# Optimization experiments

Hardware: AMD Instinct MI355X
Metric: run time of the kernel (lower is better)

The kernel has to match this reference:

```python
import jax, jax.numpy as jnp
import numpy as np

NUM_HEADS = 8
NUM_POINTS = 4


def _grid_sample_bilinear(img, grid, H, W):
    """torch F.grid_sample(mode='bilinear', padding='zeros', align_corners=False).
    img:  [B, H, W, D]   grid: [B, S, 2] with (x, y) in [-1, 1].
    Returns [B, S, D].
    """
    gx, gy = grid[..., 0], grid[..., 1]
    # align_corners=False pixel mapping
    x = ((gx + 1.0) * W - 1.0) * 0.5
    y = ((gy + 1.0) * H - 1.0) * 0.5
    x0 = jnp.floor(x)
    y0 = jnp.floor(y)
    wx1 = x - x0
    wy1 = y - y0
    x0i = x0.astype(jnp.int32)
    y0i = y0.astype(jnp.int32)
    img_flat = img.reshape(img.shape[0], H * W, img.shape[-1])  # [B, N, D]

    def corner(xi, yi, w):
        valid = (xi >= 0) & (xi < W) & (yi >= 0) & (yi < H)  # zeros padding
        idx = jnp.clip(yi, 0, H - 1) * W + jnp.clip(xi, 0, W - 1)  # [B, S]
        v = jnp.take_along_axis(img_flat, idx[..., None], axis=1)  # [B, S, D]
        return v * (w * valid.astype(img.dtype))[..., None]

    out = corner(x0i, y0i, (1.0 - wx1) * (1.0 - wy1))
    out += corner(x0i + 1, y0i, wx1 * (1.0 - wy1))
    out += corner(x0i, y0i + 1, (1.0 - wx1) * wy1)
    out += corner(x0i + 1, y0i + 1, wx1 * wy1)
    return out


def setup_inputs() -> dict:
    key = jax.random.key(0)
    ks = jax.random.split(key, 12)
    B, Q, D = 4, 1024, 256
    H, W = 128, 128
    nh, npts = NUM_HEADS, NUM_POINTS
    f32 = jnp.float32
    return {
        "query": jax.random.normal(ks[0], (B, Q, D), f32),
        "reference_points": jax.random.uniform(ks[1], (B, Q, 2), f32),
        "value": jax.random.normal(ks[2], (B, H * W, D), f32),
        "W_off": jax.random.normal(ks[3], (D, nh * npts * 2), f32) * 0.02,
        "b_off": jax.random.normal(ks[4], (nh * npts * 2,), f32) * 0.02,
        "W_attn": jax.random.normal(ks[5], (D, nh * npts), f32) * 0.02,
        "b_attn": jax.random.normal(ks[6], (nh * npts,), f32) * 0.02,
        "W_v": jax.random.normal(ks[7], (D, D), f32) * (D ** -0.5),
        "b_v": jnp.zeros((D,), f32),
        "W_out": jax.random.normal(ks[8], (nh * D, D), f32) * ((nh * D) ** -0.5),
        "b_out": jnp.zeros((D,), f32),
        "H": H,
        "W": W,
    }


def reference(query, reference_points, value, W_off, b_off, W_attn, b_attn,
              W_v, b_v, W_out, b_out, H, W):
    B, Q, D = query.shape
    nh, npts = NUM_HEADS, NUM_POINTS
    # learned offsets and per-point attention weights
    offsets = (query @ W_off + b_off).reshape(B, Q, nh, npts, 2)
    attn = jax.nn.softmax((query @ W_attn + b_attn).reshape(B, Q, nh, npts), axis=-1)
    # sampling locations in [-1, 1]
    locs = reference_points[:, :, None, None, :] + offsets * 0.1
    locs = jnp.clip(locs, 0.0, 1.0) * 2.0 - 1.0
    # value projection -> 2D feature map [B, H, W, D]
    img = (value @ W_v + b_v).reshape(B, H, W, D)
    # sample all heads/points at once
    grid = locs.reshape(B, Q * nh * npts, 2)
    sampled = _grid_sample_bilinear(img, grid, H, W).reshape(B, Q, nh, npts, D)
    # weighted reduce over points, concat heads
    weighted = jnp.einsum("bqhpd,bqhp->bqhd", sampled, attn)
    out = weighted.reshape(B, Q, nh * D) @ W_out + b_out
    return out
```

## Files before the change

### kernel.cpp

```cpp
#include <hip/hip_runtime.h>
#include <hip/hip_bf16.h>
#include <math.h>

constexpr int B  = 4;
constexpr int Q  = 1024;
constexpr int D  = 256;
constexpr int NH = 8;
constexpr int NP = 4;
constexpr int H  = 128;
constexpr int W  = 128;
constexpr int HW = H * W;
constexpr int KAUG = 2112;

typedef short   bf16x8  __attribute__((ext_vector_type(8)));
typedef float   f32x4   __attribute__((ext_vector_type(4)));
typedef short   short4v __attribute__((ext_vector_type(4)));
typedef unsigned short ushort8v __attribute__((ext_vector_type(8)));

__device__ inline unsigned short f2bf(float f) {
    union { float f; unsigned u; } v; v.f = f;
    unsigned r = v.u + 0x7fff + ((v.u >> 16) & 1);
    return (unsigned short)(r >> 16);
}
__device__ inline float bf2f(unsigned short s) {
    union { unsigned u; float f; } v; v.u = ((unsigned)s) << 16;
    return v.f;
}

__device__ inline void async16(const void* g, void* l) {
    __builtin_amdgcn_global_load_lds(
        (const __attribute__((address_space(1))) unsigned*)g,
        (__attribute__((address_space(3))) unsigned*)l, 16, 0, 0);
}

constexpr int RB_CONV  = 0;
constexpr int RB_OFF   = RB_CONV  + (B * HW * D) / 1024;
constexpr int RB_CONVT = RB_OFF   + B * Q;
constexpr int RB_WV    = RB_CONVT + (NH * D * D) / 256;
constexpr int RB_BV    = RB_WV    + (D * D) / 1024;
constexpr int RB_END   = RB_BV    + (D * 64) / 256;

__global__ __launch_bounds__(256)
void k_prep(const float* __restrict__ value,
            const float* __restrict__ query,
            const float* __restrict__ refpts,
            const float* __restrict__ W_off,  const float* __restrict__ b_off,
            const float* __restrict__ W_attn, const float* __restrict__ b_attn,
            const float* __restrict__ b_v,    const float* __restrict__ W_out,
            const float* __restrict__ W_v,
            unsigned short* __restrict__ val_bf,
            int* __restrict__ ctab,
            float* __restrict__ wtab,
            unsigned short* __restrict__ sv,
            unsigned short* __restrict__ Wout_t,
            unsigned short* __restrict__ Wv_bf,
            unsigned short* __restrict__ WcT) {
    const int blk = blockIdx.x;
    const int tid = threadIdx.x;

    if (blk < RB_OFF) {
        const int i = (blk * 1024) + tid * 4;
        const float4 v = *(const float4*)&value[i];
        short4v o;
        o.x = (short)f2bf(v.x); o.y = (short)f2bf(v.y);
        o.z = (short)f2bf(v.z); o.w = (short)f2bf(v.w);
        *(short4v*)&val_bf[i] = o;
    } else if (blk < RB_CONVT) {
        const int bq = blk - RB_OFF;
        __shared__ float qrow[D];
        __shared__ float s_loc[64];
        __shared__ float s_logit[NH * NP];
        __shared__ float s_wgt[NH * NP][4];

        qrow[tid] = query[(size_t)bq * D + tid];
        __syncthreads();

        if (tid < 64) {
            float acc = b_off[tid];
            #pragma unroll 8
            for (int k = 0; k < D; ++k) acc += qrow[k] * W_off[k * 64 + tid];
            const float ref = refpts[(size_t)bq * 2 + (tid & 1)];
            float loc = ref + acc * 0.1f;
            s_loc[tid] = fminf(fmaxf(loc, 0.0f), 1.0f) * 2.0f - 1.0f;
        } else if (tid < 96) {
            const int j = tid - 64;
            float acc = b_attn[j];
            #pragma unroll 8
            for (int k = 0; k < D; ++k) acc += qrow[k] * W_attn[k * 32 + j];
            s_logit[j] = acc;
        }
        __syncthreads();

        if (tid < NH * NP) {
            const int h = tid >> 2;
            float m = -1e30f;
            #pragma unroll
            for (int p = 0; p < NP; ++p) m = fmaxf(m, s_logit[h * NP + p]);
            float s = 0.0f;
            #pragma unroll
            for (int p = 0; p < NP; ++p) s += __expf(s_logit[h * NP + p] - m);
            const float a = __expf(s_logit[tid] - m) / s;

            const float gx = s_loc[tid * 2 + 0];
            const float gy = s_loc[tid * 2 + 1];
            const float x  = ((gx + 1.0f) * (float)W - 1.0f) * 0.5f;
            const float y  = ((gy + 1.0f) * (float)H - 1.0f) * 0.5f;
            const float x0f = floorf(x), y0f = floorf(y);
            const float wx1 = x - x0f,  wy1 = y - y0f;
            const float wx0 = 1.0f - wx1, wy0 = 1.0f - wy1;
            const int x0 = (int)x0f, y0 = (int)y0f;
            const int x1 = x0 + 1,  y1 = y0 + 1;
            const float vx0 = (x0 >= 0 && x0 < W) ? 1.0f : 0.0f;
            const float vx1 = (x1 >= 0 && x1 < W) ? 1.0f : 0.0f;
            const float vy0 = (y0 >= 0 && y0 < H) ? 1.0f : 0.0f;
            const float vy1 = (y1 >= 0 && y1 < H) ? 1.0f : 0.0f;
            const int xc0 = min(max(x0, 0), W - 1);
            const int xc1 = min(max(x1, 0), W - 1);
            const int yc0 = min(max(y0, 0), H - 1);
            const int yc1 = min(max(y1, 0), H - 1);
            int   offs[4];
            float wgts[4];
            offs[0] = yc0 * W + xc0;  wgts[0] = a * wx0 * wy0 * vx0 * vy0;
            offs[1] = yc0 * W + xc1;  wgts[1] = a * wx1 * wy0 * vx1 * vy0;
            offs[2] = yc1 * W + xc0;  wgts[2] = a * wx0 * wy1 * vx0 * vy1;
            offs[3] = yc1 * W + xc1;  wgts[3] = a * wx1 * wy1 * vx1 * vy1;
            #pragma unroll
            for (int c = 0; c < 4; ++c) {
                ctab[(size_t)bq * 128 + tid * 4 + c] = offs[c];
                wtab[(size_t)bq * 128 + tid * 4 + c] = wgts[c];
                s_wgt[tid][c] = wgts[c];
            }
        }
        __syncthreads();

        if (tid < 8) {
            float S = 0.0f;
            #pragma unroll
            for (int p = 0; p < NP; ++p)
                #pragma unroll
                for (int c = 0; c < 4; ++c) S += s_wgt[tid * 4 + p][c];
            sv[(size_t)bq * KAUG + 2048 + tid] = f2bf(S);
        } else if (tid < 64) {
            sv[(size_t)bq * KAUG + 2048 + tid] = 0;
        }
    } else if (blk < RB_WV) {
        const int i = (blk - RB_CONVT) * 256 + tid;
        const int n = i >> 11, k = i & 2047;
        Wout_t[i] = f2bf(W_out[(size_t)k * D + n]);
    } else if (blk < RB_BV) {
        const int i = (blk - RB_WV) * 1024 + tid * 4;
        const float4 v = *(const float4*)&W_v[i];
        short4v o;
        o.x = (short)f2bf(v.x); o.y = (short)f2bf(v.y);
        o.z = (short)f2bf(v.z); o.w = (short)f2bf(v.w);
        *(short4v*)&Wv_bf[i] = o;
    } else {
        const int t = (blk - RB_BV) * 256 + tid;
        const int n = t >> 6, c = t & 63;
        float v = 0.0f;
        if (c < 8) {
            #pragma unroll 8
            for (int j = 0; j < D; ++j)
                v += b_v[j] * W_out[((size_t)c * D + j) * D + n];
        }
        WcT[(size_t)n * KAUG + 2048 + c] = f2bf(v);
    }
}

template <int OUTMODE>
__global__ __launch_bounds__(256)
void k_gemm64(const unsigned short* __restrict__ A, int lda,
              const unsigned short* __restrict__ Bt, int ldb,
              const float* __restrict__ bias,
              void* __restrict__ Cout, int ldc, int K) {
    __shared__ __align__(16) unsigned short lds[4][4096];

    const int tid  = threadIdx.x;
    const int lane = tid & 63;
    const int w    = tid >> 6;
    const int wm   = w >> 1, wn = w & 1;
    const int m0 = blockIdx.x * 64, n0 = blockIdx.y * 64;
    if (OUTMODE == 1) Bt += (size_t)blockIdx.z * 256;

    const int srow = w * 8 + (lane >> 3);
    const int schk = (lane & 7) ^ (lane >> 3);
    const unsigned short* ag0 = A  + (size_t)(m0 + srow)      * lda + schk * 8;
    const unsigned short* ag1 = A  + (size_t)(m0 + srow + 32) * lda + schk * 8;
    const unsigned short* bg0 = Bt + (size_t)(n0 + srow)      * ldb + schk * 8;
    const unsigned short* bg1 = Bt + (size_t)(n0 + srow + 32) * ldb + schk * 8;
    const int l0 = w * 512 + lane * 8;
    const int l1 = l0 + 2048;

    int aoff[2][2], boff[2][2];
    #pragma unroll
    for (int i = 0; i < 2; ++i)
        #pragma unroll
        for (int kk = 0; kk < 2; ++kk) {
            const int ar = wm * 32 + i * 16 + (lane & 15);
            aoff[i][kk] = ar * 64 + ((((lane >> 4) + kk * 4) ^ (ar & 7)) * 8);
            const int br = wn * 32 + i * 16 + (lane & 15);
            boff[i][kk] = br * 64 + ((((lane >> 4) + kk * 4) ^ (br & 7)) * 8);
        }

    f32x4 acc[2][2];
    #pragma unroll
    for (int i = 0; i < 2; ++i)
        #pragma unroll
        for (int j = 0; j < 2; ++j) acc[i][j] = (f32x4){0.f, 0.f, 0.f, 0.f};

    async16(ag0, &lds[0][l0]); async16(ag1, &lds[0][l1]);
    async16(bg0, &lds[1][l0]); async16(bg1, &lds[1][l1]);

    const int niter = K >> 6;
    for (int it = 0; it < niter; ++it) {
        __syncthreads();
        const int cur = (it & 1) * 2;
        if (it + 1 < niter) {
            const int nxt = 2 - cur;
            const int ko  = (it + 1) * 64;
            async16(ag0 + ko, &lds[nxt][l0]);
            async16(ag1 + ko, &lds[nxt][l1]);
            async16(bg0 + ko, &lds[nxt + 1][l0]);
            async16(bg1 + ko, &lds[nxt + 1][l1]);
        }
        bf16x8 af[2][2], bfv[2][2];
        #pragma unroll
        for (int i = 0; i < 2; ++i)
            #pragma unroll
            for (int kk = 0; kk < 2; ++kk) {
                af[i][kk]  = *(const bf16x8*)&lds[cur][aoff[i][kk]];
                bfv[i][kk] = *(const bf16x8*)&lds[cur + 1][boff[i][kk]];
            }
        #pragma unroll
        for (int i = 0; i < 2; ++i)
            #pragma unroll
            for (int j = 0; j < 2; ++j)
                #pragma unroll
                for (int kk = 0; kk < 2; ++kk)
                    acc[i][j] = __builtin_amdgcn_mfma_f32_16x16x32_bf16(
                        af[i][kk], bfv[j][kk], acc[i][j], 0, 0, 0);
    }

    const int colb = n0 + wn * 32 + (lane & 15);
    const int rowb = m0 + wm * 32 + (lane >> 4) * 4;
    if (OUTMODE == 0) {
        float* C = (float*)Cout;
        #pragma unroll
        for (int j = 0; j < 2; ++j) {
            const int col = colb + j * 16;
            const float bb = bias[col];
            #pragma unroll
            for (int i = 0; i < 2; ++i)
                #pragma unroll
                for (int r = 0; r < 4; ++r)
                    C[(size_t)(rowb + i * 16 + r) * ldc + col] = acc[i][j][r] + bb;
        }
    } else {
        unsigned short* Wt = (unsigned short*)Cout;
        const int ocol = blockIdx.z * 256;
        #pragma unroll
        for (int j = 0; j < 2; ++j) {
            const int col = colb + j * 16;
            #pragma unroll
            for (int i = 0; i < 2; ++i)
                #pragma unroll
                for (int r = 0; r < 4; ++r)
                    Wt[(size_t)col * ldc + ocol + rowb + i * 16 + r] =
                        f2bf(acc[i][j][r]);
        }
    }
}

__global__ __launch_bounds__(256)
void k_sample(const unsigned short* __restrict__ val,
              const int* __restrict__ ctab,
              const float* __restrict__ wtab,
              unsigned short* __restrict__ sv) {
    const int bq   = blockIdx.x;
    const int b    = bq >> 10;
    const int tid  = threadIdx.x;
    const int lane = tid & 63;
    const int w    = tid >> 6;

    __shared__ int   s_off[128];
    __shared__ float s_wgt[128];
    if (tid < 128) {
        s_off[tid] = ctab[(size_t)bq * 128 + tid];
        s_wgt[tid] = wtab[(size_t)bq * 128 + tid];
    }
    __syncthreads();

    const int half = lane >> 5;
    const int l5   = lane & 31;
    const unsigned short* ib = val + (size_t)b * HW * D + l5 * 8;

    float acc[2][8] = {};
    #pragma unroll
    for (int g = 0; g < 2; ++g) {
        ushort8v vb[8];
        float    wg[8];
        #pragma unroll
        for (int j = 0; j < 8; ++j) {
            const int flat = w * 32 + (g * 8 + j) * 2 + half;
            wg[j] = s_wgt[flat];
            vb[j] = *(const ushort8v*)(ib + (size_t)s_off[flat] * D);
        }
        #pragma unroll
        for (int j = 0; j < 8; ++j)
            #pragma unroll
            for (int k = 0; k < 8; ++k)
                acc[g][k] += wg[j] * bf2f(vb[j][k]);
    }

    #pragma unroll
    for (int hh = 0; hh < 2; ++hh) {
        float comb[8];
        #pragma unroll
        for (int k = 0; k < 8; ++k)
            comb[k] = acc[hh][k] + __shfl_xor(acc[hh][k], 32, 64);
        if (half == 0) {
            const int h = w * 2 + hh;
            ushort8v o;
            #pragma unroll
            for (int k = 0; k < 8; ++k) o[k] = f2bf(comb[k]);
            *(ushort8v*)&sv[(size_t)bq * KAUG + h * D + l5 * 8] = o;
        }
    }
}

extern "C" void kernel_launch(void* const* d_in, const int* in_sizes, int n_in,
                              void* d_out, int out_size, void* d_ws, size_t ws_size,
                              hipStream_t stream) {
    const float* query  = (const float*)d_in[0];
    const float* refpts = (const float*)d_in[1];
    const float* value  = (const float*)d_in[2];
    const float* W_off  = (const float*)d_in[3];
    const float* b_off  = (const float*)d_in[4];
    const float* W_attn = (const float*)d_in[5];
    const float* b_attn = (const float*)d_in[6];
    const float* W_v    = (const float*)d_in[7];
    const float* b_v    = (const float*)d_in[8];
    const float* W_out  = (const float*)d_in[9];
    const float* b_out  = (const float*)d_in[10];
    float* out = (float*)d_out;

    char* wsb = (char*)d_ws;
    unsigned short* val_bf = (unsigned short*)(wsb);
    unsigned short* sv     = (unsigned short*)(wsb + 33554432);
    unsigned short* WcT    = (unsigned short*)(wsb + 50855936);
    unsigned short* Wout_t = (unsigned short*)(wsb + 51937280);
    unsigned short* Wv_bf  = (unsigned short*)(wsb + 52985856);
    int*            ctab   = (int*)(wsb + 53116928);
    float*          wtab   = (float*)(wsb + 55214080);

    k_prep<<<RB_END, 256, 0, stream>>>(value, query, refpts, W_off, b_off,
                                       W_attn, b_attn, b_v, W_out, W_v,
                                       val_bf, ctab, wtab, sv, Wout_t, Wv_bf, WcT);

    {
        dim3 grid(D / 64, D / 64, NH);
        k_gemm64<1><<<grid, 256, 0, stream>>>(Wv_bf, D, Wout_t, NH * D,
                                              nullptr, WcT, KAUG, D);
    }

    k_sample<<<B * Q, 256, 0, stream>>>(val_bf, ctab, wtab, sv);

    {
        dim3 grid((B * Q) / 64, D / 64, 1);
        k_gemm64<0><<<grid, 256, 0, stream>>>(sv, KAUG, WcT, KAUG,
                                              b_out, out, D, KAUG);
    }
}
```

Measured before the change: 203.5 us.

## Compute offset/attention projection with tiled SGEMM and fuse sampling setup into k_sample

Result: faster. 197.2 us (-3.1%).

```diff
diff --git a/kernel.cpp b/kernel.cpp
--- a/kernel.cpp
+++ b/kernel.cpp
@@ -34,114 +34,48 @@
 }
 
 constexpr int RB_CONV  = 0;
-constexpr int RB_OFF   = RB_CONV  + (B * HW * D) / 1024;
-constexpr int RB_CONVT = RB_OFF   + B * Q;
+constexpr int RB_WOA   = RB_CONV  + (B * HW * D) / 1024;
+constexpr int RB_BIAS  = RB_WOA   + (D * 128) / 256;
+constexpr int RB_CONVT = RB_BIAS  + 1;
 constexpr int RB_WV    = RB_CONVT + (NH * D * D) / 256;
 constexpr int RB_BV    = RB_WV    + (D * D) / 1024;
 constexpr int RB_END   = RB_BV    + (D * 64) / 256;
 
 __global__ __launch_bounds__(256)
 void k_prep(const float* __restrict__ value,
-            const float* __restrict__ query,
-            const float* __restrict__ refpts,
             const float* __restrict__ W_off,  const float* __restrict__ b_off,
             const float* __restrict__ W_attn, const float* __restrict__ b_attn,
             const float* __restrict__ b_v,    const float* __restrict__ W_out,
             const float* __restrict__ W_v,
             unsigned short* __restrict__ val_bf,
-            int* __restrict__ ctab,
-            float* __restrict__ wtab,
-            unsigned short* __restrict__ sv,
+            float* __restrict__ Woa,
+            float* __restrict__ bias_oa,
             unsigned short* __restrict__ Wout_t,
             unsigned short* __restrict__ Wv_bf,
             unsigned short* __restrict__ WcT) {
     const int blk = blockIdx.x;
     const int tid = threadIdx.x;
 
-    if (blk < RB_OFF) {
+    if (blk < RB_WOA) {
         const int i = (blk * 1024) + tid * 4;
         const float4 v = *(const float4*)&value[i];
         short4v o;
         o.x = (short)f2bf(v.x); o.y = (short)f2bf(v.y);
         o.z = (short)f2bf(v.z); o.w = (short)f2bf(v.w);
         *(short4v*)&val_bf[i] = o;
+    } else if (blk < RB_BIAS) {
+        const int i = (blk - RB_WOA) * 256 + tid;
+        const int k = i >> 7, j = i & 127;
+        float v = 0.0f;
+        if (j < 64)      v = W_off[k * 64 + j];
+        else if (j < 96) v = W_attn[k * 32 + (j - 64)];
+        Woa[i] = v;
     } else if (blk < RB_CONVT) {
-        const int bq = blk - RB_OFF;
-        __shared__ float qrow[D];
-        __shared__ float s_loc[64];
-        __shared__ float s_logit[NH * NP];
-        __shared__ float s_wgt[NH * NP][4];
-
-        qrow[tid] = query[(size_t)bq * D + tid];
-        __syncthreads();
-
-        if (tid < 64) {
-            float acc = b_off[tid];
-            #pragma unroll 8
-            for (int k = 0; k < D; ++k) acc += qrow[k] * W_off[k * 64 + tid];
-            const float ref = refpts[(size_t)bq * 2 + (tid & 1)];
-            float loc = ref + acc * 0.1f;
-            s_loc[tid] = fminf(fmaxf(loc, 0.0f), 1.0f) * 2.0f - 1.0f;
-        } else if (tid < 96) {
-            const int j = tid - 64;
-            float acc = b_attn[j];
-            #pragma unroll 8
-            for (int k = 0; k < D; ++k) acc += qrow[k] * W_attn[k * 32 + j];
-            s_logit[j] = acc;
-        }
-        __syncthreads();
-
-        if (tid < NH * NP) {
-            const int h = tid >> 2;
-            float m = -1e30f;
-            #pragma unroll
-            for (int p = 0; p < NP; ++p) m = fmaxf(m, s_logit[h * NP + p]);
-            float s = 0.0f;
-            #pragma unroll
-            for (int p = 0; p < NP; ++p) s += __expf(s_logit[h * NP + p] - m);
-            const float a = __expf(s_logit[tid] - m) / s;
-
-            const float gx = s_loc[tid * 2 + 0];
-            const float gy = s_loc[tid * 2 + 1];
-            const float x  = ((gx + 1.0f) * (float)W - 1.0f) * 0.5f;
-            const float y  = ((gy + 1.0f) * (float)H - 1.0f) * 0.5f;
-            const float x0f = floorf(x), y0f = floorf(y);
-            const float wx1 = x - x0f,  wy1 = y - y0f;
-            const float wx0 = 1.0f - wx1, wy0 = 1.0f - wy1;
-            const int x0 = (int)x0f, y0 = (int)y0f;
-            const int x1 = x0 + 1,  y1 = y0 + 1;
-            const float vx0 = (x0 >= 0 && x0 < W) ? 1.0f : 0.0f;
-            const float vx1 = (x1 >= 0 && x1 < W) ? 1.0f : 0.0f;
-            const float vy0 = (y0 >= 0 && y0 < H) ? 1.0f : 0.0f;
-            const float vy1 = (y1 >= 0 && y1 < H) ? 1.0f : 0.0f;
-            const int xc0 = min(max(x0, 0), W - 1);
-            const int xc1 = min(max(x1, 0), W - 1);
-            const int yc0 = min(max(y0, 0), H - 1);
-            const int yc1 = min(max(y1, 0), H - 1);
-            int   offs[4];
-            float wgts[4];
-            offs[0] = yc0 * W + xc0;  wgts[0] = a * wx0 * wy0 * vx0 * vy0;
-            offs[1] = yc0 * W + xc1;  wgts[1] = a * wx1 * wy0 * vx1 * vy0;
-            offs[2] = yc1 * W + xc0;  wgts[2] = a * wx0 * wy1 * vx0 * vy1;
-            offs[3] = yc1 * W + xc1;  wgts[3] = a * wx1 * wy1 * vx1 * vy1;
-            #pragma unroll
-            for (int c = 0; c < 4; ++c) {
-                ctab[(size_t)bq * 128 + tid * 4 + c] = offs[c];
-                wtab[(size_t)bq * 128 + tid * 4 + c] = wgts[c];
-                s_wgt[tid][c] = wgts[c];
-            }
-        }
-        __syncthreads();
-
-        if (tid < 8) {
-            float S = 0.0f;
-            #pragma unroll
-            for (int p = 0; p < NP; ++p)
-                #pragma unroll
-                for (int c = 0; c < 4; ++c) S += s_wgt[tid * 4 + p][c];
-            sv[(size_t)bq * KAUG + 2048 + tid] = f2bf(S);
-        } else if (tid < 64) {
-            sv[(size_t)bq * KAUG + 2048 + tid] = 0;
+        if (tid < 128) {
+            float v = 0.0f;
+            if (tid < 64)      v = b_off[tid];
+            else if (tid < 96) v = b_attn[tid - 64];
+            bias_oa[tid] = v;
         }
     } else if (blk < RB_WV) {
         const int i = (blk - RB_CONVT) * 256 + tid;
@@ -167,6 +101,65 @@
     }
 }
 
+#define BM 64
+#define BN 64
+#define BK 16
+
+__global__ __launch_bounds__(256)
+void k_sgemm(const float* __restrict__ A, const float* __restrict__ Bm,
+             const float* __restrict__ bias, float* __restrict__ C,
+             int M, int N, int K) {
+    __shared__ __align__(16) float As[BK][BM + 4];
+    __shared__ __align__(16) float Bs[BK][BN + 4];
+
+    const int t  = threadIdx.x;
+    const int tx = t & 15;
+    const int ty = t >> 4;
+    const int m0 = blockIdx.x * BM;
+    const int n0 = blockIdx.y * BN;
+
+    const int arow = t >> 2;
+    const int akg  = (t & 3) * 4;
+    const int brow = t >> 4;
+    const int bcol = (t & 15) * 4;
+
+    float acc[4][4] = {};
+
+    for (int k0 = 0; k0 < K; k0 += BK) {
+        const float4 av = *(const float4*)&A[(size_t)(m0 + arow) * K + k0 + akg];
+        const float4 bv = *(const float4*)&Bm[(size_t)(k0 + brow) * N + n0 + bcol];
+        __syncthreads();
+        As[akg + 0][arow] = av.x;
+        As[akg + 1][arow] = av.y;
+        As[akg + 2][arow] = av.z;
+        As[akg + 3][arow] = av.w;
+        *(float4*)&Bs[brow][bcol] = bv;
+        __syncthreads();
+
+        #pragma unroll
+        for (int kk = 0; kk < BK; ++kk) {
+            const float4 a = *(const float4*)&As[kk][ty * 4];
+            const float4 b = *(const float4*)&Bs[kk][tx * 4];
+            acc[0][0] += a.x * b.x; acc[0][1] += a.x * b.y; acc[0][2] += a.x * b.z; acc[0][3] += a.x * b.w;
+            acc[1][0] += a.y * b.x; acc[1][1] += a.y * b.y; acc[1][2] += a.y * b.z; acc[1][3] += a.y * b.w;
+            acc[2][0] += a.z * b.x; acc[2][1] += a.z * b.y; acc[2][2] += a.z * b.z; acc[2][3] += a.z * b.w;
+            acc[3][0] += a.w * b.x; acc[3][1] += a.w * b.y; acc[3][2] += a.w * b.z; acc[3][3] += a.w * b.w;
+        }
+    }
+
+    const float4 bb = *(const float4*)&bias[n0 + tx * 4];
+    #pragma unroll
+    for (int i = 0; i < 4; ++i) {
+        const int m = m0 + ty * 4 + i;
+        float4 r;
+        r.x = acc[i][0] + bb.x;
+        r.y = acc[i][1] + bb.y;
+        r.z = acc[i][2] + bb.z;
+        r.w = acc[i][3] + bb.w;
+        *(float4*)&C[(size_t)m * N + n0 + tx * 4] = r;
+    }
+}
+
 template <int OUTMODE>
 __global__ __launch_bounds__(256)
 void k_gemm64(const unsigned short* __restrict__ A, int lda,
@@ -273,8 +266,8 @@
 
 __global__ __launch_bounds__(256)
 void k_sample(const unsigned short* __restrict__ val,
-              const int* __restrict__ ctab,
-              const float* __restrict__ wtab,
+              const float* __restrict__ raw,
+              const float* __restrict__ refpts,
               unsigned short* __restrict__ sv) {
     const int bq   = blockIdx.x;
     const int b    = bq >> 10;
@@ -282,13 +275,61 @@
     const int lane = tid & 63;
     const int w    = tid >> 6;
 
+    __shared__ float s_raw[128];
     __shared__ int   s_off[128];
     __shared__ float s_wgt[128];
-    if (tid < 128) {
-        s_off[tid] = ctab[(size_t)bq * 128 + tid];
-        s_wgt[tid] = wtab[(size_t)bq * 128 + tid];
-    }
+
+    if (tid < 128) s_raw[tid] = raw[(size_t)bq * 128 + tid];
     __syncthreads();
+
+    if (tid < NH * NP) {
+        const int h = tid >> 2;
+        float m = -1e30f;
+        #pragma unroll
+        for (int p = 0; p < NP; ++p) m = fmaxf(m, s_raw[64 + h * 4 + p]);
+        float s = 0.0f;
+        #pragma unroll
+        for (int p = 0; p < NP; ++p) s += __expf(s_raw[64 + h * 4 + p] - m);
+        const float a = __expf(s_raw[64 + tid] - m) / s;
+
+        const float refx = refpts[(size_t)bq * 2 + 0];
+        const float refy = refpts[(size_t)bq * 2 + 1];
+        const float gx = fminf(fmaxf(refx + s_raw[tid * 2 + 0] * 0.1f, 0.0f), 1.0f) * 2.0f - 1.0f;
+        const float gy = fminf(fmaxf(refy + s_raw[tid * 2 + 1] * 0.1f, 0.0f), 1.0f) * 2.0f - 1.0f;
+        const float x  = ((gx + 1.0f) * (float)W - 1.0f) * 0.5f;
+        const float y  = ((gy + 1.0f) * (float)H - 1.0f) * 0.5f;
+        const float x0f = floorf(x), y0f = floorf(y);
+        const float wx1 = x - x0f,  wy1 = y - y0f;
+        const float wx0 = 1.0f - wx1, wy0 = 1.0f - wy1;
+        const int x0 = (int)x0f, y0 = (int)y0f;
+        const int x1 = x0 + 1,  y1 = y0 + 1;
+        const float vx0 = (x0 >= 0 && x0 < W) ? 1.0f : 0.0f;
+        const float vx1 = (x1 >= 0 && x1 < W) ? 1.0f : 0.0f;
+        const float vy0 = (y0 >= 0 && y0 < H) ? 1.0f : 0.0f;
+        const float vy1 = (y1 >= 0 && y1 < H) ? 1.0f : 0.0f;
+        const int xc0 = min(max(x0, 0), W - 1);
+        const int xc1 = min(max(x1, 0), W - 1);
+        const int yc0 = min(max(y0, 0), H - 1);
+        const int yc1 = min(max(y1, 0), H - 1);
+        s_off[tid * 4 + 0] = yc0 * W + xc0;
+        s_off[tid * 4 + 1] = yc0 * W + xc1;
+        s_off[tid * 4 + 2] = yc1 * W + xc0;
+        s_off[tid * 4 + 3] = yc1 * W + xc1;
+        s_wgt[tid * 4 + 0] = a * wx0 * wy0 * vx0 * vy0;
+        s_wgt[tid * 4 + 1] = a * wx1 * wy0 * vx1 * vy0;
+        s_wgt[tid * 4 + 2] = a * wx0 * wy1 * vx0 * vy1;
+        s_wgt[tid * 4 + 3] = a * wx1 * wy1 * vx1 * vy1;
+    }
+    __syncthreads();
+
+    if (tid < 8) {
+        float S = 0.0f;
+        #pragma unroll
+        for (int c = 0; c < 16; ++c) S += s_wgt[tid * 16 + c];
+        sv[(size_t)bq * KAUG + 2048 + tid] = f2bf(S);
+    } else if (tid < 64) {
+        sv[(size_t)bq * KAUG + 2048 + tid] = 0;
+    }
 
     const int half = lane >> 5;
     const int l5   = lane & 31;
@@ -345,17 +386,24 @@
     float* out = (float*)d_out;
 
     char* wsb = (char*)d_ws;
-    unsigned short* val_bf = (unsigned short*)(wsb);
-    unsigned short* sv     = (unsigned short*)(wsb + 33554432);
-    unsigned short* WcT    = (unsigned short*)(wsb + 50855936);
-    unsigned short* Wout_t = (unsigned short*)(wsb + 51937280);
-    unsigned short* Wv_bf  = (unsigned short*)(wsb + 52985856);
-    int*            ctab   = (int*)(wsb + 53116928);
-    float*          wtab   = (float*)(wsb + 55214080);
-
-    k_prep<<<RB_END, 256, 0, stream>>>(value, query, refpts, W_off, b_off,
-                                       W_attn, b_attn, b_v, W_out, W_v,
-                                       val_bf, ctab, wtab, sv, Wout_t, Wv_bf, WcT);
+    unsigned short* val_bf  = (unsigned short*)(wsb);
+    unsigned short* sv      = (unsigned short*)(wsb + 33554432);
+    unsigned short* WcT     = (unsigned short*)(wsb + 50855936);
+    unsigned short* Wout_t  = (unsigned short*)(wsb + 51937280);
+    unsigned short* Wv_bf   = (unsigned short*)(wsb + 52985856);
+    float*          raw     = (float*)(wsb + 53116928);
+    float*          Woa     = (float*)(wsb + 55214080);
+    float*          bias_oa = (float*)(wsb + 55345152);
+
+    k_prep<<<RB_END, 256, 0, stream>>>(value, W_off, b_off, W_attn, b_attn,
+                                       b_v, W_out, W_v,
+                                       val_bf, Woa, bias_oa, Wout_t, Wv_bf, WcT);
+
+    {
+        dim3 grid((B * Q) / BM, 128 / BN);
+        k_sgemm<<<grid, 256, 0, stream>>>(query, Woa, bias_oa, raw,
+                                          B * Q, 128, D);
+    }
 
     {
         dim3 grid(D / 64, D / 64, NH);
@@ -363,7 +411,7 @@
                                               nullptr, WcT, KAUG, D);
     }
 
-    k_sample<<<B * Q, 256, 0, stream>>>(val_bf, ctab, wtab, sv);
+    k_sample<<<B * Q, 256, 0, stream>>>(val_bf, raw, refpts, sv);
 
     {
         dim3 grid((B * Q) / 64, D / 64, 1);
```
